# Optimization experiments

Measured on AMD Instinct MI355X. Metric: run time of the kernel, lower is better.

## Reference

```python
import jax, jax.numpy as jnp
import numpy as np

INPUT_DIM = 256
N_NODES = 100000
N_EDGES = 500000


def setup_inputs() -> dict:
    key = jax.random.key(0)
    ks = jax.random.split(key, 10)
    d = INPUT_DIM

    def linear(kw, kb, fan_in, fan_out):
        # torch nn.Linear default init: U(-1/sqrt(fan_in), 1/sqrt(fan_in))
        bound = 1.0 / np.sqrt(fan_in)
        W = jax.random.uniform(kw, (fan_out, fan_in), jnp.float32, -bound, bound)
        b = jax.random.uniform(kb, (fan_out,), jnp.float32, -bound, bound)
        return W, b

    W1, b1 = linear(ks[0], ks[1], 2 * d, 2 * d)
    W2, b2 = linear(ks[2], ks[3], 2 * d, d)
    W3, b3 = linear(ks[4], ks[5], d, d)
    W4, b4 = linear(ks[6], ks[7], d, 1)

    z = jax.random.normal(ks[8], (N_NODES, d), jnp.float32)
    edge_index = jax.random.randint(ks[9], (2, N_EDGES), 0, N_NODES, jnp.int64)
    return {
        "z": z, "edge_index": edge_index,
        "W1": W1, "b1": b1, "W2": W2, "b2": b2,
        "W3": W3, "b3": b3, "W4": W4, "b4": b4,
    }


def reference(z, edge_index, W1, b1, W2, b2, W3, b3, W4, b4):
    row, col = edge_index[0], edge_index[1]
    # gather endpoint embeddings and concat: [E, 2d]
    z_concat = jnp.concatenate([z[row], z[col]], axis=1)
    # dropout is identity in eval mode (reference runs deterministic)
    x = jax.nn.relu(z_concat @ W1.T + b1)
    x = jax.nn.relu(x @ W2.T + b2)
    x = jax.nn.relu(x @ W3.T + b3)
    return jax.nn.sigmoid(x @ W4.T + b4)  # [E, 1]
```

## Files before the change

kernel.cpp:

```cpp
#include <hip/hip_runtime.h>
#include <math.h>


typedef _Float16 f16x8 __attribute__((ext_vector_type(8)));
typedef _Float16 f16x4 __attribute__((ext_vector_type(4)));
typedef float    f32x4 __attribute__((ext_vector_type(4)));

#define W1E (512*512)
#define W2E (256*512)
#define W3E (256*256)
#define WTOT (W1E+W2E+W3E)
#define H_OFF 1048576

__global__ void repack_w(const float* __restrict__ W1, const float* __restrict__ W2,
                         const float* __restrict__ W3, _Float16* __restrict__ wout) {
  int t = blockIdx.x * 256 + threadIdx.x;
  if (t >= WTOT) return;
  const float* src; _Float16* dst; int K, idx;
  if (t < W1E)            { src = W1; K = 512; idx = t;             dst = wout; }
  else if (t < W1E + W2E) { src = W2; K = 512; idx = t - W1E;       dst = wout + W1E; }
  else                    { src = W3; K = 256; idx = t - (W1E+W2E); dst = wout + W1E + W2E; }
  int j    = idx & 7;
  int lane = (idx >> 3) & 63;
  int rest = idx >> 9;
  int ktiles = K >> 5;
  int kt = rest % ktiles;
  int nt = rest / ktiles;
  int n = nt * 16 + (lane & 15);
  int k = kt * 32 + (lane >> 4) * 8 + j;
  dst[idx] = (_Float16)src[n * K + k];
}

__global__ __launch_bounds__(512, 2)
void precompute_h(const float* __restrict__ z, int N, const float* __restrict__ b1,
                  const _Float16* __restrict__ w1, _Float16* __restrict__ H) {
  __shared__ char smem[32768];
  const int tid  = threadIdx.x;
  const int wid  = tid >> 6;
  const int lane = tid & 63;
  const int l15  = lane & 15;
  const int lhi  = lane >> 4;
  const int nbase = blockIdx.x * 64;
  const int cb    = blockIdx.y;

  for (int r = wid; r < 64; r += 8) {
    int n = nbase + r; if (n >= N) n = N - 1;
    float4 v = *(const float4*)(z + (size_t)n * 256 + lane * 4);
    f16x4 h;
    h[0] = (_Float16)v.x; h[1] = (_Float16)v.y; h[2] = (_Float16)v.z; h[3] = (_Float16)v.w;
    *(f16x4*)(smem + r * 512 + ((lane * 8) ^ ((r & 7) << 4))) = h;
  }
  __syncthreads();

  f32x4 acc[4][4];
  #pragma unroll
  for (int nt = 0; nt < 4; ++nt) {
    f32x4 bv = (f32x4){0.f, 0.f, 0.f, 0.f};
    if (cb == 0) bv = *(const f32x4*)(b1 + wid*64 + nt*16 + lhi*4);
    #pragma unroll
    for (int et = 0; et < 4; ++et) acc[nt][et] = bv;
  }

  for (int kt = 0; kt < 8; ++kt) {
    int ktw = kt + cb * 8;
    f16x8 wf[4], xf[4];
    #pragma unroll
    for (int nt = 0; nt < 4; ++nt)
      wf[nt] = *(const f16x8*)(w1 + (((wid*4 + nt)*16 + ktw)*64 + lane) * 8);
    #pragma unroll
    for (int et = 0; et < 4; ++et) {
      int r = et*16 + l15;
      xf[et] = *(const f16x8*)(smem + r * 512 + ((kt*64 + lhi*16) ^ ((r & 7) << 4)));
    }
    #pragma unroll
    for (int nt = 0; nt < 4; ++nt)
      #pragma unroll
      for (int et = 0; et < 4; ++et)
        acc[nt][et] = __builtin_amdgcn_mfma_f32_16x16x32_f16(wf[nt], xf[et], acc[nt][et], 0, 0, 0);
  }

  #pragma unroll
  for (int nt = 0; nt < 4; ++nt)
    #pragma unroll
    for (int et = 0; et < 4; ++et) {
      int n = nbase + et*16 + l15;
      if (n < N) {
        f16x4 h;
        #pragma unroll
        for (int r = 0; r < 4; ++r) h[r] = (_Float16)acc[nt][et][r];
        *(f16x4*)(H + (size_t)n * 1024 + cb*512 + wid*64 + nt*16 + lhi*4) = h;
      }
    }
}

#define SCR_OFF  65536
#define BIAS_OFF 67584
#define LDS2_BYTES (BIAS_OFF + 3080)

__global__ __launch_bounds__(512, 4)
void fused_edges(const int* __restrict__ ei, int E, const _Float16* __restrict__ H,
                 const float* __restrict__ b2, const float* __restrict__ b3,
                 const float* __restrict__ W4, const float* __restrict__ b4,
                 const _Float16* __restrict__ w2, const _Float16* __restrict__ w3,
                 float* __restrict__ out) {
  extern __shared__ char smem[];
  float* scr = (float*)(smem + SCR_OFF);
  float* bls = (float*)(smem + BIAS_OFF);

  const int tid  = threadIdx.x;
  const int wid  = tid >> 6;
  const int lane = tid & 63;
  const int l15  = lane & 15;
  const int lhi  = lane >> 4;
  const int base = blockIdx.x * 64;

  for (int i = tid; i < 769; i += 512) {
    float v;
    if (i < 256)      v = b2[i];
    else if (i < 512) v = b3[i - 256];
    else if (i < 768) v = W4[i - 512];
    else              v = b4[0];
    bls[i] = v;
  }

  #pragma unroll 4
  for (int e8 = 0; e8 < 8; ++e8) {
    int e = e8 * 8 + wid;
    int ge = base + e; if (ge >= E) ge = E - 1;
    int nr = ei[ge];
    int nc = ei[E + ge];
    f16x8 ha = *(const f16x8*)(H + (size_t)nr * 1024 + lane * 8);
    f16x8 hb = *(const f16x8*)(H + (size_t)nc * 1024 + 512 + lane * 8);
    f16x8 s = ha + hb;
    #pragma unroll
    for (int j = 0; j < 8; ++j) s[j] = (s[j] > (_Float16)0) ? s[j] : (_Float16)0;
    *(f16x8*)(smem + e * 1024 + ((lane * 16) ^ ((e & 7) << 4))) = s;
  }
  __syncthreads();

  f32x4 acc2[2][4];
  #pragma unroll
  for (int nt = 0; nt < 2; ++nt) {
    f32x4 bv = *(const f32x4*)(bls + wid*32 + nt*16 + lhi*4);
    #pragma unroll
    for (int et = 0; et < 4; ++et) acc2[nt][et] = bv;
  }
  for (int kt = 0; kt < 16; ++kt) {
    f16x8 wf[2], xf[4];
    #pragma unroll
    for (int nt = 0; nt < 2; ++nt)
      wf[nt] = *(const f16x8*)(w2 + (((wid*2 + nt)*16 + kt)*64 + lane) * 8);
    #pragma unroll
    for (int et = 0; et < 4; ++et) {
      int e = et*16 + l15;
      xf[et] = *(const f16x8*)(smem + e * 1024 + ((kt*64 + lhi*16) ^ ((e & 7) << 4)));
    }
    #pragma unroll
    for (int nt = 0; nt < 2; ++nt)
      #pragma unroll
      for (int et = 0; et < 4; ++et)
        acc2[nt][et] = __builtin_amdgcn_mfma_f32_16x16x32_f16(wf[nt], xf[et], acc2[nt][et], 0, 0, 0);
  }
  __syncthreads();
  #pragma unroll
  for (int nt = 0; nt < 2; ++nt)
    #pragma unroll
    for (int et = 0; et < 4; ++et) {
      int e = et*16 + l15;
      int ncb = (wid*32 + nt*16 + lhi*4) * 2;
      f16x4 h;
      #pragma unroll
      for (int r = 0; r < 4; ++r) h[r] = (_Float16)fmaxf(acc2[nt][et][r], 0.f);
      *(f16x4*)(smem + e * 512 + (ncb ^ ((e & 7) << 4))) = h;
    }
  __syncthreads();

  f32x4 acc3[2][4];
  #pragma unroll
  for (int nt = 0; nt < 2; ++nt) {
    f32x4 bv = *(const f32x4*)(bls + 256 + wid*32 + nt*16 + lhi*4);
    #pragma unroll
    for (int et = 0; et < 4; ++et) acc3[nt][et] = bv;
  }
  for (int kt = 0; kt < 8; ++kt) {
    f16x8 wf[2], xf[4];
    #pragma unroll
    for (int nt = 0; nt < 2; ++nt)
      wf[nt] = *(const f16x8*)(w3 + (((wid*2 + nt)*8 + kt)*64 + lane) * 8);
    #pragma unroll
    for (int et = 0; et < 4; ++et) {
      int e = et*16 + l15;
      xf[et] = *(const f16x8*)(smem + e * 512 + ((kt*64 + lhi*16) ^ ((e & 7) << 4)));
    }
    #pragma unroll
    for (int nt = 0; nt < 2; ++nt)
      #pragma unroll
      for (int et = 0; et < 4; ++et)
        acc3[nt][et] = __builtin_amdgcn_mfma_f32_16x16x32_f16(wf[nt], xf[et], acc3[nt][et], 0, 0, 0);
  }

  f32x4 w4v[2];
  #pragma unroll
  for (int nt = 0; nt < 2; ++nt)
    w4v[nt] = *(const f32x4*)(bls + 512 + wid*32 + nt*16 + lhi*4);
  float bias4 = bls[768];

  #pragma unroll
  for (int et = 0; et < 4; ++et) {
    float p = 0.f;
    #pragma unroll
    for (int nt = 0; nt < 2; ++nt)
      #pragma unroll
      for (int r = 0; r < 4; ++r)
        p += fmaxf(acc3[nt][et][r], 0.f) * w4v[nt][r];
    p += __shfl_xor(p, 16);
    p += __shfl_xor(p, 32);
    if (lane < 16) scr[(et*16 + l15) * 8 + wid] = p;
  }
  __syncthreads();

  if (tid < 64) {
    int ge = base + tid;
    if (ge < E) {
      float s = bias4;
      #pragma unroll
      for (int w = 0; w < 8; ++w) s += scr[tid*8 + w];
      out[ge] = 1.f / (1.f + expf(-s));
    }
  }
}

#define FSCR_OFF  65536
#define FBIAS_OFF 67584
#define FLDS_BYTES 72832

__global__ __launch_bounds__(512, 2)
void fused_fallback(const float* __restrict__ z, const int* __restrict__ ei, int E,
                    const float* __restrict__ b1, const float* __restrict__ b2,
                    const float* __restrict__ b3, const float* __restrict__ W4,
                    const float* __restrict__ b4,
                    const _Float16* __restrict__ wbuf, float* __restrict__ out) {
  extern __shared__ char smem[];
  float* scr = (float*)(smem + FSCR_OFF);
  float* bls = (float*)(smem + FBIAS_OFF);

  const int tid  = threadIdx.x;
  const int wid  = tid >> 6;
  const int lane = tid & 63;
  const int l15  = lane & 15;
  const int lhi  = lane >> 4;
  const int base = blockIdx.x * 64;

  for (int i = tid; i < 1281; i += 512) {
    float v;
    if (i < 512)       v = b1[i];
    else if (i < 768)  v = b2[i - 512];
    else if (i < 1024) v = b3[i - 768];
    else if (i < 1280) v = W4[i - 1024];
    else               v = b4[0];
    bls[i] = v;
  }

  for (int it = wid; it < 128; it += 8) {
    int e = it >> 1, half = it & 1;
    int ge = base + e; if (ge >= E) ge = E - 1;
    int src = ei[half ? (E + ge) : ge];
    float4 v = *(const float4*)(z + (size_t)src * 256 + lane * 4);
    f16x4 h;
    h[0] = (_Float16)v.x; h[1] = (_Float16)v.y; h[2] = (_Float16)v.z; h[3] = (_Float16)v.w;
    *(f16x4*)(smem + e * 1024 + ((half * 512 + lane * 8) ^ ((e & 7) << 4))) = h;
  }
  __syncthreads();

  const _Float16* w1 = wbuf;
  const _Float16* w2 = wbuf + W1E;
  const _Float16* w3 = wbuf + W1E + W2E;

  f32x4 acc1[4][4];
  #pragma unroll
  for (int nt = 0; nt < 4; ++nt) {
    f32x4 bv = *(const f32x4*)(bls + wid*64 + nt*16 + lhi*4);
    #pragma unroll
    for (int et = 0; et < 4; ++et) acc1[nt][et] = bv;
  }
  for (int kt = 0; kt < 16; ++kt) {
    f16x8 wf[4], xf[4];
    #pragma unroll
    for (int nt = 0; nt < 4; ++nt)
      wf[nt] = *(const f16x8*)(w1 + (((wid*4 + nt)*16 + kt)*64 + lane) * 8);
    #pragma unroll
    for (int et = 0; et < 4; ++et) {
      int e = et*16 + l15;
      xf[et] = *(const f16x8*)(smem + e * 1024 + ((kt*64 + lhi*16) ^ ((e & 7) << 4)));
    }
    #pragma unroll
    for (int nt = 0; nt < 4; ++nt)
      #pragma unroll
      for (int et = 0; et < 4; ++et)
        acc1[nt][et] = __builtin_amdgcn_mfma_f32_16x16x32_f16(wf[nt], xf[et], acc1[nt][et], 0, 0, 0);
  }
  __syncthreads();
  #pragma unroll
  for (int nt = 0; nt < 4; ++nt)
    #pragma unroll
    for (int et = 0; et < 4; ++et) {
      int e = et*16 + l15;
      int ncb = (wid*64 + nt*16 + lhi*4) * 2;
      f16x4 h;
      #pragma unroll
      for (int r = 0; r < 4; ++r) h[r] = (_Float16)fmaxf(acc1[nt][et][r], 0.f);
      *(f16x4*)(smem + e * 1024 + (ncb ^ ((e & 7) << 4))) = h;
    }
  __syncthreads();

  f32x4 acc2[2][4];
  #pragma unroll
  for (int nt = 0; nt < 2; ++nt) {
    f32x4 bv = *(const f32x4*)(bls + 512 + wid*32 + nt*16 + lhi*4);
    #pragma unroll
    for (int et = 0; et < 4; ++et) acc2[nt][et] = bv;
  }
  for (int kt = 0; kt < 16; ++kt) {
    f16x8 wf[2], xf[4];
    #pragma unroll
    for (int nt = 0; nt < 2; ++nt)
      wf[nt] = *(const f16x8*)(w2 + (((wid*2 + nt)*16 + kt)*64 + lane) * 8);
    #pragma unroll
    for (int et = 0; et < 4; ++et) {
      int e = et*16 + l15;
      xf[et] = *(const f16x8*)(smem + e * 1024 + ((kt*64 + lhi*16) ^ ((e & 7) << 4)));
    }
    #pragma unroll
    for (int nt = 0; nt < 2; ++nt)
      #pragma unroll
      for (int et = 0; et < 4; ++et)
        acc2[nt][et] = __builtin_amdgcn_mfma_f32_16x16x32_f16(wf[nt], xf[et], acc2[nt][et], 0, 0, 0);
  }
  __syncthreads();
  #pragma unroll
  for (int nt = 0; nt < 2; ++nt)
    #pragma unroll
    for (int et = 0; et < 4; ++et) {
      int e = et*16 + l15;
      int ncb = (wid*32 + nt*16 + lhi*4) * 2;
      f16x4 h;
      #pragma unroll
      for (int r = 0; r < 4; ++r) h[r] = (_Float16)fmaxf(acc2[nt][et][r], 0.f);
      *(f16x4*)(smem + e * 512 + (ncb ^ ((e & 7) << 4))) = h;
    }
  __syncthreads();

  f32x4 acc3[2][4];
  #pragma unroll
  for (int nt = 0; nt < 2; ++nt) {
    f32x4 bv = *(const f32x4*)(bls + 768 + wid*32 + nt*16 + lhi*4);
    #pragma unroll
    for (int et = 0; et < 4; ++et) acc3[nt][et] = bv;
  }
  for (int kt = 0; kt < 8; ++kt) {
    f16x8 wf[2], xf[4];
    #pragma unroll
    for (int nt = 0; nt < 2; ++nt)
      wf[nt] = *(const f16x8*)(w3 + (((wid*2 + nt)*8 + kt)*64 + lane) * 8);
    #pragma unroll
    for (int et = 0; et < 4; ++et) {
      int e = et*16 + l15;
      xf[et] = *(const f16x8*)(smem + e * 512 + ((kt*64 + lhi*16) ^ ((e & 7) << 4)));
    }
    #pragma unroll
    for (int nt = 0; nt < 2; ++nt)
      #pragma unroll
      for (int et = 0; et < 4; ++et)
        acc3[nt][et] = __builtin_amdgcn_mfma_f32_16x16x32_f16(wf[nt], xf[et], acc3[nt][et], 0, 0, 0);
  }

  f32x4 w4v[2];
  #pragma unroll
  for (int nt = 0; nt < 2; ++nt)
    w4v[nt] = *(const f32x4*)(bls + 1024 + wid*32 + nt*16 + lhi*4);
  float bias4 = bls[1280];

  #pragma unroll
  for (int et = 0; et < 4; ++et) {
    float p = 0.f;
    #pragma unroll
    for (int nt = 0; nt < 2; ++nt)
      #pragma unroll
      for (int r = 0; r < 4; ++r)
        p += fmaxf(acc3[nt][et][r], 0.f) * w4v[nt][r];
    p += __shfl_xor(p, 16);
    p += __shfl_xor(p, 32);
    if (lane < 16) scr[(et*16 + l15) * 8 + wid] = p;
  }
  __syncthreads();

  if (tid < 64) {
    int ge = base + tid;
    if (ge < E) {
      float s = bias4;
      #pragma unroll
      for (int w = 0; w < 8; ++w) s += scr[tid*8 + w];
      out[ge] = 1.f / (1.f + expf(-s));
    }
  }
}

extern "C" void kernel_launch(void* const* d_in, const int* in_sizes, int n_in,
                              void* d_out, int out_size, void* d_ws, size_t ws_size,
                              hipStream_t stream) {
  const float* z  = (const float*)d_in[0];
  const int*   ei = (const int*)d_in[1];
  const float* W1 = (const float*)d_in[2];
  const float* b1 = (const float*)d_in[3];
  const float* W2 = (const float*)d_in[4];
  const float* b2 = (const float*)d_in[5];
  const float* W3 = (const float*)d_in[6];
  const float* b3 = (const float*)d_in[7];
  const float* W4 = (const float*)d_in[8];
  const float* b4 = (const float*)d_in[9];
  float* out = (float*)d_out;
  const int E = in_sizes[1] / 2;
  const int N = in_sizes[0] / 256;

  _Float16* wbuf = (_Float16*)d_ws;
  _Float16* H    = (_Float16*)((char*)d_ws + H_OFF);

  repack_w<<<(WTOT + 255) / 256, 256, 0, stream>>>(W1, W2, W3, wbuf);

  size_t need = (size_t)H_OFF + (size_t)N * 1024 * 2;
  int nblk = (E + 63) / 64;
  if (ws_size >= need) {
    dim3 pg((N + 63) / 64, 2);
    precompute_h<<<pg, 512, 0, stream>>>(z, N, b1, wbuf, H);
    fused_edges<<<nblk, 512, LDS2_BYTES, stream>>>(ei, E, H, b2, b3, W4, b4,
                                                   wbuf + W1E, wbuf + W1E + W2E, out);
  } else {
    fused_fallback<<<nblk, 512, FLDS_BYTES, stream>>>(z, ei, E, b1, b2, b3, W4, b4, wbuf, out);
  }
}
```

Before: 450.3 us.

## Merge precompute column halves into one block and shrink edge tile to 48

The node precompute kernel now handles both K-halves of W1 inside one block: four warps take each half and loop over two column passes, so each z tile is loaded and converted once instead of twice. The edge kernel now processes 48 edges per block instead of 64, which cuts LDS use to 48KB. Biases and W4 are read straight from global memory rather than staged in LDS, and the launch bounds are raised to 6 blocks per CU to increase occupancy. In exchange, each block does less MFMA work per weight fragment it loads, so weight reuse drops.

```diff
diff --git a/kernel.cpp b/kernel.cpp
--- a/kernel.cpp
+++ b/kernel.cpp
@@ -31,9 +31,9 @@
   dst[idx] = (_Float16)src[n * K + k];
 }
 
-__global__ __launch_bounds__(512, 2)
-void precompute_h(const float* __restrict__ z, int N, const float* __restrict__ b1,
-                  const _Float16* __restrict__ w1, _Float16* __restrict__ H) {
+__global__ __launch_bounds__(512, 4)
+void precompute_h2(const float* __restrict__ z, int N, const float* __restrict__ b1,
+                   const _Float16* __restrict__ w1, _Float16* __restrict__ H) {
   __shared__ char smem[32768];
   const int tid  = threadIdx.x;
   const int wid  = tid >> 6;
@@ -41,7 +41,8 @@
   const int l15  = lane & 15;
   const int lhi  = lane >> 4;
   const int nbase = blockIdx.x * 64;
-  const int cb    = blockIdx.y;
+  const int half = wid >> 2;
+  const int wloc = wid & 3;
 
   for (int r = wid; r < 64; r += 8) {
     int n = nbase + r; if (n >= N) n = N - 1;
@@ -52,80 +53,72 @@
   }
   __syncthreads();
 
-  f32x4 acc[4][4];
-  #pragma unroll
-  for (int nt = 0; nt < 4; ++nt) {
-    f32x4 bv = (f32x4){0.f, 0.f, 0.f, 0.f};
-    if (cb == 0) bv = *(const f32x4*)(b1 + wid*64 + nt*16 + lhi*4);
-    #pragma unroll
-    for (int et = 0; et < 4; ++et) acc[nt][et] = bv;
-  }
-
-  for (int kt = 0; kt < 8; ++kt) {
-    int ktw = kt + cb * 8;
-    f16x8 wf[4], xf[4];
+  for (int p = 0; p < 2; ++p) {
+    f32x4 acc[4][4];
+    #pragma unroll
+    for (int nt = 0; nt < 4; ++nt) {
+      f32x4 bv = (f32x4){0.f, 0.f, 0.f, 0.f};
+      if (half == 0) bv = *(const f32x4*)(b1 + wloc*128 + p*64 + nt*16 + lhi*4);
+      #pragma unroll
+      for (int et = 0; et < 4; ++et) acc[nt][et] = bv;
+    }
+
+    for (int kt = 0; kt < 8; ++kt) {
+      int ktg = kt + half * 8;
+      f16x8 wf[4], xf[4];
+      #pragma unroll
+      for (int nt = 0; nt < 4; ++nt) {
+        int ntg = wloc*8 + p*4 + nt;
+        wf[nt] = *(const f16x8*)(w1 + (((ntg*16 + ktg)*64 + lane)) * 8);
+      }
+      #pragma unroll
+      for (int et = 0; et < 4; ++et) {
+        int r = et*16 + l15;
+        xf[et] = *(const f16x8*)(smem + r * 512 + ((kt*64 + lhi*16) ^ ((r & 7) << 4)));
+      }
+      #pragma unroll
+      for (int nt = 0; nt < 4; ++nt)
+        #pragma unroll
+        for (int et = 0; et < 4; ++et)
+          acc[nt][et] = __builtin_amdgcn_mfma_f32_16x16x32_f16(wf[nt], xf[et], acc[nt][et], 0, 0, 0);
+    }
+
     #pragma unroll
     for (int nt = 0; nt < 4; ++nt)
-      wf[nt] = *(const f16x8*)(w1 + (((wid*4 + nt)*16 + ktw)*64 + lane) * 8);
-    #pragma unroll
-    for (int et = 0; et < 4; ++et) {
-      int r = et*16 + l15;
-      xf[et] = *(const f16x8*)(smem + r * 512 + ((kt*64 + lhi*16) ^ ((r & 7) << 4)));
-    }
-    #pragma unroll
-    for (int nt = 0; nt < 4; ++nt)
-      #pragma unroll
-      for (int et = 0; et < 4; ++et)
-        acc[nt][et] = __builtin_amdgcn_mfma_f32_16x16x32_f16(wf[nt], xf[et], acc[nt][et], 0, 0, 0);
-  }
-
-  #pragma unroll
-  for (int nt = 0; nt < 4; ++nt)
-    #pragma unroll
-    for (int et = 0; et < 4; ++et) {
-      int n = nbase + et*16 + l15;
-      if (n < N) {
-        f16x4 h;
-        #pragma unroll
-        for (int r = 0; r < 4; ++r) h[r] = (_Float16)acc[nt][et][r];
-        *(f16x4*)(H + (size_t)n * 1024 + cb*512 + wid*64 + nt*16 + lhi*4) = h;
+      #pragma unroll
+      for (int et = 0; et < 4; ++et) {
+        int n = nbase + et*16 + l15;
+        if (n < N) {
+          f16x4 h;
+          #pragma unroll
+          for (int r = 0; r < 4; ++r) h[r] = (_Float16)acc[nt][et][r];
+          *(f16x4*)(H + (size_t)n * 1024 + half*512 + wloc*128 + p*64 + nt*16 + lhi*4) = h;
+        }
       }
-    }
+  }
 }
 
-#define SCR_OFF  65536
-#define BIAS_OFF 67584
-#define LDS2_BYTES (BIAS_OFF + 3080)
-
-__global__ __launch_bounds__(512, 4)
-void fused_edges(const int* __restrict__ ei, int E, const _Float16* __restrict__ H,
-                 const float* __restrict__ b2, const float* __restrict__ b3,
-                 const float* __restrict__ W4, const float* __restrict__ b4,
-                 const _Float16* __restrict__ w2, const _Float16* __restrict__ w3,
-                 float* __restrict__ out) {
+#define SCR_OFF  24576
+#define LDS2_BYTES 49152
+
+__global__ __launch_bounds__(512, 6)
+void fused_edges48(const int* __restrict__ ei, int E, const _Float16* __restrict__ H,
+                   const float* __restrict__ b2, const float* __restrict__ b3,
+                   const float* __restrict__ W4, const float* __restrict__ b4,
+                   const _Float16* __restrict__ w2, const _Float16* __restrict__ w3,
+                   float* __restrict__ out) {
   extern __shared__ char smem[];
   float* scr = (float*)(smem + SCR_OFF);
-  float* bls = (float*)(smem + BIAS_OFF);
 
   const int tid  = threadIdx.x;
   const int wid  = tid >> 6;
   const int lane = tid & 63;
   const int l15  = lane & 15;
   const int lhi  = lane >> 4;
-  const int base = blockIdx.x * 64;
-
-  for (int i = tid; i < 769; i += 512) {
-    float v;
-    if (i < 256)      v = b2[i];
-    else if (i < 512) v = b3[i - 256];
-    else if (i < 768) v = W4[i - 512];
-    else              v = b4[0];
-    bls[i] = v;
-  }
-
-  #pragma unroll 4
-  for (int e8 = 0; e8 < 8; ++e8) {
-    int e = e8 * 8 + wid;
+  const int base = blockIdx.x * 48;
+
+  #pragma unroll 3
+  for (int e = wid; e < 48; e += 8) {
     int ge = base + e; if (ge >= E) ge = E - 1;
     int nr = ei[ge];
     int nc = ei[E + ge];
@@ -138,34 +131,34 @@
   }
   __syncthreads();
 
-  f32x4 acc2[2][4];
+  f32x4 acc2[2][3];
   #pragma unroll
   for (int nt = 0; nt < 2; ++nt) {
-    f32x4 bv = *(const f32x4*)(bls + wid*32 + nt*16 + lhi*4);
-    #pragma unroll
-    for (int et = 0; et < 4; ++et) acc2[nt][et] = bv;
+    f32x4 bv = *(const f32x4*)(b2 + wid*32 + nt*16 + lhi*4);
+    #pragma unroll
+    for (int et = 0; et < 3; ++et) acc2[nt][et] = bv;
   }
   for (int kt = 0; kt < 16; ++kt) {
-    f16x8 wf[2], xf[4];
+    f16x8 wf[2], xf[3];
     #pragma unroll
     for (int nt = 0; nt < 2; ++nt)
       wf[nt] = *(const f16x8*)(w2 + (((wid*2 + nt)*16 + kt)*64 + lane) * 8);
     #pragma unroll
-    for (int et = 0; et < 4; ++et) {
+    for (int et = 0; et < 3; ++et) {
       int e = et*16 + l15;
       xf[et] = *(const f16x8*)(smem + e * 1024 + ((kt*64 + lhi*16) ^ ((e & 7) << 4)));
     }
     #pragma unroll
     for (int nt = 0; nt < 2; ++nt)
       #pragma unroll
-      for (int et = 0; et < 4; ++et)
+      for (int et = 0; et < 3; ++et)
         acc2[nt][et] = __builtin_amdgcn_mfma_f32_16x16x32_f16(wf[nt], xf[et], acc2[nt][et], 0, 0, 0);
   }
   __syncthreads();
   #pragma unroll
   for (int nt = 0; nt < 2; ++nt)
     #pragma unroll
-    for (int et = 0; et < 4; ++et) {
+    for (int et = 0; et < 3; ++et) {
       int e = et*16 + l15;
       int ncb = (wid*32 + nt*16 + lhi*4) * 2;
       f16x4 h;
@@ -175,38 +168,37 @@
     }
   __syncthreads();
 
-  f32x4 acc3[2][4];
+  f32x4 acc3[2][3];
   #pragma unroll
   for (int nt = 0; nt < 2; ++nt) {
-    f32x4 bv = *(const f32x4*)(bls + 256 + wid*32 + nt*16 + lhi*4);
-    #pragma unroll
-    for (int et = 0; et < 4; ++et) acc3[nt][et] = bv;
+    f32x4 bv = *(const f32x4*)(b3 + wid*32 + nt*16 + lhi*4);
+    #pragma unroll
+    for (int et = 0; et < 3; ++et) acc3[nt][et] = bv;
   }
   for (int kt = 0; kt < 8; ++kt) {
-    f16x8 wf[2], xf[4];
+    f16x8 wf[2], xf[3];
     #pragma unroll
     for (int nt = 0; nt < 2; ++nt)
       wf[nt] = *(const f16x8*)(w3 + (((wid*2 + nt)*8 + kt)*64 + lane) * 8);
     #pragma unroll
-    for (int et = 0; et < 4; ++et) {
+    for (int et = 0; et < 3; ++et) {
       int e = et*16 + l15;
       xf[et] = *(const f16x8*)(smem + e * 512 + ((kt*64 + lhi*16) ^ ((e & 7) << 4)));
     }
     #pragma unroll
     for (int nt = 0; nt < 2; ++nt)
       #pragma unroll
-      for (int et = 0; et < 4; ++et)
+      for (int et = 0; et < 3; ++et)
         acc3[nt][et] = __builtin_amdgcn_mfma_f32_16x16x32_f16(wf[nt], xf[et], acc3[nt][et], 0, 0, 0);
   }
 
   f32x4 w4v[2];
   #pragma unroll
   for (int nt = 0; nt < 2; ++nt)
-    w4v[nt] = *(const f32x4*)(bls + 512 + wid*32 + nt*16 + lhi*4);
-  float bias4 = bls[768];
-
-  #pragma unroll
-  for (int et = 0; et < 4; ++et) {
+    w4v[nt] = *(const f32x4*)(W4 + wid*32 + nt*16 + lhi*4);
+
+  #pragma unroll
+  for (int et = 0; et < 3; ++et) {
     float p = 0.f;
     #pragma unroll
     for (int nt = 0; nt < 2; ++nt)
@@ -219,10 +211,10 @@
   }
   __syncthreads();
 
-  if (tid < 64) {
+  if (tid < 48) {
     int ge = base + tid;
     if (ge < E) {
-      float s = bias4;
+      float s = b4[0];
       #pragma unroll
       for (int w = 0; w < 8; ++w) s += scr[tid*8 + w];
       out[ge] = 1.f / (1.f + expf(-s));
@@ -262,13 +254,13 @@
   }
 
   for (int it = wid; it < 128; it += 8) {
-    int e = it >> 1, half = it & 1;
+    int e = it >> 1, hf = it & 1;
     int ge = base + e; if (ge >= E) ge = E - 1;
-    int src = ei[half ? (E + ge) : ge];
+    int src = ei[hf ? (E + ge) : ge];
     float4 v = *(const float4*)(z + (size_t)src * 256 + lane * 4);
     f16x4 h;
     h[0] = (_Float16)v.x; h[1] = (_Float16)v.y; h[2] = (_Float16)v.z; h[3] = (_Float16)v.w;
-    *(f16x4*)(smem + e * 1024 + ((half * 512 + lane * 8) ^ ((e & 7) << 4))) = h;
+    *(f16x4*)(smem + e * 1024 + ((hf * 512 + lane * 8) ^ ((e & 7) << 4))) = h;
   }
   __syncthreads();
 
@@ -428,13 +420,13 @@
   repack_w<<<(WTOT + 255) / 256, 256, 0, stream>>>(W1, W2, W3, wbuf);
 
   size_t need = (size_t)H_OFF + (size_t)N * 1024 * 2;
-  int nblk = (E + 63) / 64;
   if (ws_size >= need) {
-    dim3 pg((N + 63) / 64, 2);
-    precompute_h<<<pg, 512, 0, stream>>>(z, N, b1, wbuf, H);
-    fused_edges<<<nblk, 512, LDS2_BYTES, stream>>>(ei, E, H, b2, b3, W4, b4,
-                                                   wbuf + W1E, wbuf + W1E + W2E, out);
+    precompute_h2<<<(N + 63) / 64, 512, 0, stream>>>(z, N, b1, wbuf, H);
+    int nblk = (E + 47) / 48;
+    fused_edges48<<<nblk, 512, LDS2_BYTES, stream>>>(ei, E, H, b2, b3, W4, b4,
+                                                     wbuf + W1E, wbuf + W1E + W2E, out);
   } else {
+    int nblk = (E + 63) / 64;
     fused_fallback<<<nblk, 512, FLDS_BYTES, stream>>>(z, ei, E, b1, b2, b3, W4, b4, wbuf, out);
   }
 }
```

Result: slower. 583.1 us (+29.5%).
